# Kernel tuning notes

Hardware: AMD Instinct MI355X
Metric: run time of the kernel (lower is better)

## Reference

```python
import jax, jax.numpy as jnp
import numpy as np

B, C, H, W = 32, 1536, 24, 24
HID, D, K = 512, 128, 64  # hidden, cluster_dim, num_clusters


def setup_inputs() -> dict:
    key = jax.random.key(0)
    ks = jax.random.split(key, 6)
    def rn(k, shape, scale):
        return jax.random.normal(k, shape, dtype=jnp.float32) * scale
    return {
        "x": rn(ks[0], (B, C, H, W), 1.0),
        # cluster_features: Conv2d(C,512,1) -> ReLU -> Conv2d(512,D,1)
        "w1c": rn(ks[1], (HID, C), 0.02), "b1c": jnp.zeros((HID,), jnp.float32),
        "w2c": rn(ks[2], (D, HID), 0.02), "b2c": jnp.zeros((D,), jnp.float32),
        # score: Conv2d(C,512,1) -> ReLU -> Conv2d(512,K,1)
        "w1s": rn(ks[3], (HID, C), 0.02), "b1s": jnp.zeros((HID,), jnp.float32),
        "w2s": rn(ks[4], (K, HID), 0.02), "b2s": jnp.zeros((K,), jnp.float32),
        "temperature": jnp.array(1.0, jnp.float32),
    }


def _sinkhorn_log(S, num_iters=3):
    # log-domain OT solver with uniform marginals log(1/n), reg=1 (M/reg == M)
    b, m, n = S.shape
    norm = -jnp.log(jnp.asarray(n, S.dtype))
    log_a = jnp.full((b, m), norm, S.dtype)
    log_b = jnp.full((b, n), norm, S.dtype)
    u = jnp.zeros((b, m), S.dtype)
    v = jnp.zeros((b, n), S.dtype)
    for _ in range(num_iters):
        u = log_a - jax.nn.logsumexp(S + v[:, None, :], axis=2)
        v = log_b - jax.nn.logsumexp(S + u[:, :, None], axis=1)
    # get_matching_probs subtracts norm at the end
    return S + u[:, :, None] + v[:, None, :] - norm


def reference(x, w1c, b1c, w2c, b2c, w1s, b1s, w2s, b2s, temperature):
    b, c, h, w = x.shape
    xf = x.reshape(b, c, h * w)  # (B, C, N); 1x1 conv == channel GEMM
    # cluster features f: (B, D, N)
    hc = jax.nn.relu(jnp.einsum('oc,bcn->bon', w1c, xf) + b1c[None, :, None])
    f = jnp.einsum('oc,bcn->bon', w2c, hc) + b2c[None, :, None]
    # assignment scores p: (B, K, N)
    hs = jax.nn.relu(jnp.einsum('oc,bcn->bon', w1s, xf) + b1s[None, :, None])
    s = jnp.einsum('oc,bcn->bon', w2s, hs) + b2s[None, :, None]
    log_p = _sinkhorn_log(s, num_iters=3)
    p = jnp.exp(log_p / temperature) + jnp.exp(log_p)  # (B, K, N)
    # (f.unsqueeze(2) * p.unsqueeze(1)).sum(-1) == batched matmul
    agg = jnp.einsum('bcn,bkn->bck', f, p)  # (B, D, K)
    flat = agg.reshape(b, -1)
    nrm = jnp.maximum(jnp.linalg.norm(flat, axis=-1, keepdims=True), 1e-12)
    return flat / nrm
```

## Files before the change

### kernel.cpp

```cpp
#include <hip/hip_runtime.h>

typedef unsigned short ushort_t;
typedef float f32x4 __attribute__((ext_vector_type(4)));
typedef short short8 __attribute__((ext_vector_type(8)));

#define B_   32
#define C_   1536
#define N_   576
#define HID_ 512
#define D_   128
#define K_   64

__device__ __forceinline__ float bf2f(ushort_t u) {
    union { unsigned u; float f; } c; c.u = ((unsigned)u) << 16; return c.f;
}
__device__ __forceinline__ ushort_t f2bf(float x) {
    unsigned u = __float_as_uint(x);
    return (ushort_t)((u + 0x7FFFu + ((u >> 16) & 1u)) >> 16);
}

typedef const __attribute__((address_space(1))) char gas_char;
typedef __attribute__((address_space(3))) char las_char;
__device__ __forceinline__ void cp16(const void* g, void* l) {
    __builtin_amdgcn_global_load_lds((gas_char*)(size_t)g,
                                     (las_char*)(unsigned)(size_t)l, 16, 0, 0);
}
__device__ __forceinline__ void bar() {
    asm volatile("" ::: "memory");
    __builtin_amdgcn_s_barrier();
    asm volatile("" ::: "memory");
}

#define OB1_  1572864
#define OW2C_ 1573888
#define OB2C_ 1639424
#define OW2S_ 1639552
#define OB2S_ 1672320
#define WTOT_ 1672384
#define TRB_  6912
#define CVB4_ (((WTOT_ / 4) + 255) / 256)

__global__ __launch_bounds__(256) void prep_kernel(
    const void* __restrict__ x,
    const void* __restrict__ w1c, const void* __restrict__ b1c,
    const void* __restrict__ w2c, const void* __restrict__ b2c,
    const void* __restrict__ w1s, const void* __restrict__ b1s,
    const void* __restrict__ w2s, const void* __restrict__ b2s,
    const unsigned* __restrict__ temp,
    ushort_t* __restrict__ xt, ushort_t* __restrict__ o, float* __restrict__ Tp)
{
    __shared__ ushort_t t[64][68];
    unsigned d = temp[0];
    int flag = (d == 0x3F800000u) ? 1 : 0;
    int tid = threadIdx.x;
    int idx = blockIdx.x;
    if (idx == 0 && tid == 0)
        *Tp = flag ? __uint_as_float(d) : bf2f((ushort_t)(d & 0xFFFFu));

    if (idx < TRB_) {
        int b = idx / 216, rem = idx % 216;
        int c0 = (rem % 24) * 64, n0 = (rem / 24) * 64;
        ushort_t* xtb = xt + (size_t)b * N_ * C_;
        int r = tid >> 4, c4 = (tid & 15) * 4;
        if (flag) {
            const float* xb = (const float*)x + (size_t)b * C_ * N_;
#pragma unroll
            for (int i = 0; i < 4; ++i) {
                int cc = r + i * 16;
                float4 v = *(const float4*)&xb[(size_t)(c0 + cc) * N_ + n0 + c4];
                t[cc][c4 + 0] = f2bf(v.x);
                t[cc][c4 + 1] = f2bf(v.y);
                t[cc][c4 + 2] = f2bf(v.z);
                t[cc][c4 + 3] = f2bf(v.w);
            }
        } else {
            const ushort_t* xb = (const ushort_t*)x + (size_t)b * C_ * N_;
#pragma unroll
            for (int i = 0; i < 4; ++i) {
                int cc = r + i * 16;
                *(uint2*)&t[cc][c4] =
                    *(const uint2*)&xb[(size_t)(c0 + cc) * N_ + n0 + c4];
            }
        }
        __syncthreads();
#pragma unroll
        for (int i = 0; i < 4; ++i) {
            int nn = r + i * 16;
            ushort_t v0 = t[c4 + 0][nn], v1 = t[c4 + 1][nn];
            ushort_t v2 = t[c4 + 2][nn], v3 = t[c4 + 3][nn];
            uint2 vv;
            vv.x = (unsigned)v0 | ((unsigned)v1 << 16);
            vv.y = (unsigned)v2 | ((unsigned)v3 << 16);
            *(uint2*)&xtb[(size_t)(n0 + nn) * C_ + c0 + c4] = vv;
        }
    } else {
        int i4 = ((idx - TRB_) * 256 + tid) * 4;
        if (i4 >= WTOT_) return;
        const void* p; int off;
        if      (i4 < 786432)  { p = w1c; off = i4; }
        else if (i4 < OB1_)    { p = w1s; off = i4 - 786432; }
        else if (i4 < 1573376) { p = b1c; off = i4 - OB1_; }
        else if (i4 < OW2C_)   { p = b1s; off = i4 - 1573376; }
        else if (i4 < OB2C_)   { p = w2c; off = i4 - OW2C_; }
        else if (i4 < OW2S_)   { p = b2c; off = i4 - OB2C_; }
        else if (i4 < OB2S_)   { p = w2s; off = i4 - OW2S_; }
        else                   { p = b2s; off = i4 - OB2S_; }
        if (flag) {
            float4 v = *(const float4*)((const float*)p + off);
            uint2 r;
            r.x = (unsigned)f2bf(v.x) | ((unsigned)f2bf(v.y) << 16);
            r.y = (unsigned)f2bf(v.z) | ((unsigned)f2bf(v.w) << 16);
            *(uint2*)&o[i4] = r;
        } else {
            *(uint2*)&o[i4] = *(const uint2*)((const ushort_t*)p + off);
        }
    }
}

__global__ __launch_bounds__(256) void gemm1_kernel(
    const ushort_t* __restrict__ Xt, const ushort_t* __restrict__ W1,
    const ushort_t* __restrict__ bias, ushort_t* __restrict__ h)
{
    __shared__ ushort_t Atile[2][128 * 64];
    __shared__ ushort_t Btile[2][128 * 64];
    int idx = blockIdx.x;
    int l = (idx & 7) * 144 + (idx >> 3);
    int mt = l >> 3, t = l & 7;
    int row0 = mt * 128, col0 = t * 128;

    int tid = threadIdx.x, w = tid >> 6, lane = tid & 63;
    int wr = w >> 1, wc = w & 1;
    int r16 = lane & 15, q = lane >> 4, kh = q * 8;

    int srow = tid >> 3;
    int cx = ((tid & 7) ^ (srow & 7)) * 8;
    const ushort_t* ag[4];
    const ushort_t* bg[4];
#pragma unroll
    for (int s = 0; s < 4; ++s) {
        ag[s] = Xt + (size_t)(row0 + s * 32 + srow) * C_ + cx;
        bg[s] = W1 + (size_t)(col0 + s * 32 + srow) * C_ + cx;
    }

    f32x4 acc[4][4];
#pragma unroll
    for (int i = 0; i < 4; ++i)
#pragma unroll
        for (int j = 0; j < 4; ++j) acc[i][j] = f32x4{0.f, 0.f, 0.f, 0.f};

    int rowa = wr * 64 + r16;
    int rowb = wc * 64 + r16;
    int xr = (r16 & 7) * 8;

    auto stage = [&](int buf) {
#pragma unroll
        for (int s = 0; s < 4; ++s) {
            cp16(ag[s], &Atile[buf][tid * 8 + s * 2048]);
            cp16(bg[s], &Btile[buf][tid * 8 + s * 2048]);
            ag[s] += 64; bg[s] += 64;
        }
    };
    auto compute = [&](int cb) {
#pragma unroll
        for (int ks = 0; ks < 2; ++ks) {
            int ke = (ks * 32 + kh) ^ xr;
            short8 af[4], bf[4];
#pragma unroll
            for (int i = 0; i < 4; ++i)
                af[i] = *(const short8*)&Atile[cb][(rowa + i * 16) * 64 + ke];
#pragma unroll
            for (int j = 0; j < 4; ++j)
                bf[j] = *(const short8*)&Btile[cb][(rowb + j * 16) * 64 + ke];
#pragma unroll
            for (int i = 0; i < 4; ++i)
#pragma unroll
                for (int j = 0; j < 4; ++j)
                    acc[i][j] = __builtin_amdgcn_mfma_f32_16x16x32_bf16(
                        af[i], bf[j], acc[i][j], 0, 0, 0);
        }
    };

    stage(0);
    int cur = 0;
    for (int kt = 0; kt < 23; ++kt) {
        stage(cur ^ 1);
        asm volatile("s_waitcnt vmcnt(8)" ::: "memory");
        bar();
        compute(cur);
        bar();
        cur ^= 1;
    }
    asm volatile("s_waitcnt vmcnt(0)" ::: "memory");
    bar();
    compute(cur);

#pragma unroll
    for (int j = 0; j < 4; ++j) {
        int col = col0 + wc * 64 + j * 16 + r16;
        float cb = bf2f(bias[col]);
#pragma unroll
        for (int i = 0; i < 4; ++i) {
            int rowo = row0 + wr * 64 + i * 16 + q * 4;
#pragma unroll
            for (int r = 0; r < 4; ++r) {
                float v = fmaxf(acc[i][j][r] + cb, 0.f);
                h[(size_t)(rowo + r) * 1024 + col] = f2bf(v);
            }
        }
    }
}

__global__ __launch_bounds__(256) void gemm2_kernel(
    const ushort_t* __restrict__ Wb, const ushort_t* __restrict__ h,
    ushort_t* __restrict__ fbuf, float* __restrict__ sbuf)
{
    __shared__ ushort_t Atile[2][128 * 32];
    __shared__ ushort_t Btile[2][128 * 32];
    int nt = blockIdx.x, b = blockIdx.y, z = blockIdx.z;
    int col0 = nt * 128;
    int Mclamp = z ? K_ : D_;
    const ushort_t* Aw   = Wb + (z ? OW2S_ : OW2C_);
    const ushort_t* bias = Wb + (z ? OB2S_ : OB2C_);
    const ushort_t* hb = h + (size_t)b * N_ * 1024 + (z ? 512 : 0);

    int tid = threadIdx.x, w = tid >> 6, lane = tid & 63;
    int wr = w >> 1, wc = w & 1;
    int r16 = lane & 15, q = lane >> 4, kh = q * 8;

    int srow = tid >> 2;
    int swz = ((tid & 3) ^ (srow & 3)) * 8;
    int ar0 = min(srow, Mclamp - 1);
    int ar1 = min(64 + srow, Mclamp - 1);
    const ushort_t* ag0 = Aw + (size_t)ar0 * HID_ + swz;
    const ushort_t* ag1 = Aw + (size_t)ar1 * HID_ + swz;
    int br0 = min(col0 + srow, N_ - 1);
    int br1 = min(col0 + 64 + srow, N_ - 1);
    const ushort_t* bg0 = hb + (size_t)br0 * 1024 + swz;
    const ushort_t* bg1 = hb + (size_t)br1 * 1024 + swz;

    f32x4 acc[4][4];
#pragma unroll
    for (int i = 0; i < 4; ++i)
#pragma unroll
        for (int j = 0; j < 4; ++j) acc[i][j] = f32x4{0.f, 0.f, 0.f, 0.f};

    int xr = (r16 & 3) * 8;

    auto stage = [&](int buf) {
        cp16(ag0, &Atile[buf][tid * 8]);
        cp16(ag1, &Atile[buf][2048 + tid * 8]);
        cp16(bg0, &Btile[buf][tid * 8]);
        cp16(bg1, &Btile[buf][2048 + tid * 8]);
        ag0 += 32; ag1 += 32; bg0 += 32; bg1 += 32;
    };
    auto compute = [&](int cb) {
        int ke = kh ^ xr;
        short8 af[4], bf[4];
#pragma unroll
        for (int i = 0; i < 4; ++i)
            af[i] = *(const short8*)&Atile[cb][(wr * 64 + i * 16 + r16) * 32 + ke];
#pragma unroll
        for (int j = 0; j < 4; ++j)
            bf[j] = *(const short8*)&Btile[cb][(wc * 64 + j * 16 + r16) * 32 + ke];
#pragma unroll
        for (int i = 0; i < 4; ++i)
#pragma unroll
            for (int j = 0; j < 4; ++j)
                acc[i][j] = __builtin_amdgcn_mfma_f32_16x16x32_bf16(
                    af[i], bf[j], acc[i][j], 0, 0, 0);
    };

    stage(0);
    int cur = 0;
    for (int kt = 0; kt < 15; ++kt) {
        stage(cur ^ 1);
        asm volatile("s_waitcnt vmcnt(4)" ::: "memory");
        bar();
        compute(cur);
        bar();
        cur ^= 1;
    }
    asm volatile("s_waitcnt vmcnt(0)" ::: "memory");
    bar();
    compute(cur);

#pragma unroll
    for (int j = 0; j < 4; ++j) {
        int col = col0 + wc * 64 + j * 16 + r16;
#pragma unroll
        for (int i = 0; i < 4; ++i) {
            int rowb = wr * 64 + i * 16 + q * 4;
#pragma unroll
            for (int r = 0; r < 4; ++r) {
                int rr = rowb + r;
                if (rr < Mclamp && col < N_) {
                    float v = acc[i][j][r] + bf2f(bias[rr]);
                    if (z == 0)
                        fbuf[(size_t)b * D_ * N_ + (size_t)rr * N_ + col] = f2bf(v);
                    else
                        sbuf[(size_t)b * K_ * N_ + (size_t)rr * N_ + col] = v;
                }
            }
        }
    }
}

__global__ __launch_bounds__(512) void sinkhorn_kernel(
    const float* __restrict__ s_all, const float* __restrict__ Tp,
    ushort_t* __restrict__ P_all)
{
    int b = blockIdx.x;
    const float* S = s_all + (size_t)b * K_ * N_;
    __shared__ float Sl[K_ * 577];
    __shared__ float su[K_];
    __shared__ float sv[N_];
    int tid = threadIdx.x, w = tid >> 6, lane = tid & 63;
    const float norm = -logf((float)N_);

    const float4* S4 = (const float4*)S;
    for (int g = tid; g < (K_ * N_) / 4; g += 512) {
        float4 v = S4[g];
        int w0 = g * 4;
        int r = w0 / N_;
        int base = w0 + r;
        Sl[base + 0] = v.x; Sl[base + 1] = v.y;
        Sl[base + 2] = v.z; Sl[base + 3] = v.w;
    }
    for (int n = tid; n < N_; n += 512) sv[n] = 0.f;
    __syncthreads();

    for (int it = 0; it < 3; ++it) {
        for (int r = w; r < K_; r += 8) {
            const float* Sr = Sl + r * 577;
            float a0 = 0.f, a1 = 0.f, a2 = 0.f;
#pragma unroll
            for (int k = 0; k < 9; k += 3) {
                int n0 = lane + 64 * k;
                a0 += __expf(Sr[n0] + sv[n0]);
                a1 += __expf(Sr[n0 + 64] + sv[n0 + 64]);
                a2 += __expf(Sr[n0 + 128] + sv[n0 + 128]);
            }
            float t = a0 + a1 + a2;
#pragma unroll
            for (int off = 32; off; off >>= 1) t += __shfl_xor(t, off);
            if (lane == 0) su[r] = norm - __logf(t);
        }
        __syncthreads();
        for (int n = tid; n < N_; n += 512) {
            const float* Sc = Sl + n;
            float a0 = 0.f, a1 = 0.f, a2 = 0.f, a3 = 0.f;
#pragma unroll
            for (int m = 0; m < K_; m += 4) {
                a0 += __expf(Sc[(m + 0) * 577] + su[m + 0]);
                a1 += __expf(Sc[(m + 1) * 577] + su[m + 1]);
                a2 += __expf(Sc[(m + 2) * 577] + su[m + 2]);
                a3 += __expf(Sc[(m + 3) * 577] + su[m + 3]);
            }
            sv[n] = norm - __logf((a0 + a1) + (a2 + a3));
        }
        __syncthreads();
    }

    float invT = 1.f / (*Tp);
    ushort_t* Pb = P_all + (size_t)b * K_ * N_;
    for (int r = w; r < K_; r += 8) {
        float ur = su[r];
        const float* Sr = Sl + r * 577;
#pragma unroll
        for (int k = 0; k < 9; ++k) {
            int n0 = lane + 64 * k;
            float lp = Sr[n0] + ur + sv[n0] - norm;
            Pb[r * N_ + n0] = f2bf(__expf(lp * invT) + __expf(lp));
        }
    }
}

__global__ __launch_bounds__(256) void aggnorm_kernel(
    const ushort_t* __restrict__ f_all, const ushort_t* __restrict__ P_all,
    const unsigned* __restrict__ temp, void* __restrict__ out)
{
    __shared__ ushort_t Atile[2][128 * 64];
    __shared__ ushort_t Ptile[2][64 * 64];
    __shared__ float red[4];
    int b = blockIdx.x;
    const ushort_t* F = f_all + (size_t)b * D_ * N_;
    const ushort_t* P = P_all + (size_t)b * K_ * N_;
    int tid = threadIdx.x, w = tid >> 6, lane = tid & 63;
    int wr = w >> 1, wc = w & 1;
    int r16 = lane & 15, q = lane >> 4, kh = q * 8;

    int srow = tid >> 3;
    int cx = ((tid & 7) ^ (srow & 7)) * 8;
    const ushort_t* fg[4];
    const ushort_t* pg[2];
#pragma unroll
    for (int s = 0; s < 4; ++s)
        fg[s] = F + (size_t)(s * 32 + srow) * N_ + cx;
#pragma unroll
    for (int s = 0; s < 2; ++s)
        pg[s] = P + (size_t)(s * 32 + srow) * N_ + cx;

    f32x4 acc[4][2];
#pragma unroll
    for (int i = 0; i < 4; ++i)
#pragma unroll
        for (int j = 0; j < 2; ++j) acc[i][j] = f32x4{0.f, 0.f, 0.f, 0.f};

    int rowa = wr * 64 + r16;
    int rowp = wc * 32 + r16;
    int xr = (r16 & 7) * 8;

    auto stage = [&](int buf) {
#pragma unroll
        for (int s = 0; s < 4; ++s) {
            cp16(fg[s], &Atile[buf][tid * 8 + s * 2048]);
            fg[s] += 64;
        }
#pragma unroll
        for (int s = 0; s < 2; ++s) {
            cp16(pg[s], &Ptile[buf][tid * 8 + s * 2048]);
            pg[s] += 64;
        }
    };
    auto compute = [&](int cb) {
#pragma unroll
        for (int ks = 0; ks < 2; ++ks) {
            int ke = (ks * 32 + kh) ^ xr;
            short8 af[4], pf[2];
#pragma unroll
            for (int i = 0; i < 4; ++i)
                af[i] = *(const short8*)&Atile[cb][(rowa + i * 16) * 64 + ke];
#pragma unroll
            for (int j = 0; j < 2; ++j)
                pf[j] = *(const short8*)&Ptile[cb][(rowp + j * 16) * 64 + ke];
#pragma unroll
            for (int i = 0; i < 4; ++i)
#pragma unroll
                for (int j = 0; j < 2; ++j)
                    acc[i][j] = __builtin_amdgcn_mfma_f32_16x16x32_bf16(
                        af[i], pf[j], acc[i][j], 0, 0, 0);
        }
    };

    stage(0);
    int cur = 0;
    for (int kt = 0; kt < 8; ++kt) {
        stage(cur ^ 1);
        asm volatile("s_waitcnt vmcnt(6)" ::: "memory");
        bar();
        compute(cur);
        bar();
        cur ^= 1;
    }
    asm volatile("s_waitcnt vmcnt(0)" ::: "memory");
    bar();
    compute(cur);

    float ssq = 0.f;
#pragma unroll
    for (int i = 0; i < 4; ++i)
#pragma unroll
        for (int j = 0; j < 2; ++j)
#pragma unroll
            for (int r = 0; r < 4; ++r) { float v = acc[i][j][r]; ssq += v * v; }
#pragma unroll
    for (int off = 32; off; off >>= 1) ssq += __shfl_xor(ssq, off);
    if (lane == 0) red[w] = ssq;
    __syncthreads();
    float tot = red[0] + red[1] + red[2] + red[3];
    float inv = 1.f / fmaxf(sqrtf(tot), 1e-12f);
    int flag = (temp[0] == 0x3F800000u) ? 1 : 0;
#pragma unroll
    for (int i = 0; i < 4; ++i) {
#pragma unroll
        for (int j = 0; j < 2; ++j) {
            int col = wc * 32 + j * 16 + r16;
#pragma unroll
            for (int r = 0; r < 4; ++r) {
                int row = wr * 64 + i * 16 + q * 4 + r;
                float v = acc[i][j][r] * inv;
                size_t idx = (size_t)b * D_ * K_ + (size_t)row * K_ + col;
                if (flag) ((float*)out)[idx] = v;
                else      ((ushort_t*)out)[idx] = f2bf(v);
            }
        }
    }
}

extern "C" void kernel_launch(void* const* d_in, const int* in_sizes, int n_in,
                              void* d_out, int out_size, void* d_ws, size_t ws_size,
                              hipStream_t stream) {
    const void* x    = d_in[0];
    const void* w1c  = d_in[1];
    const void* b1c  = d_in[2];
    const void* w2c  = d_in[3];
    const void* b2c  = d_in[4];
    const void* w1s  = d_in[5];
    const void* b1s  = d_in[6];
    const void* w2s  = d_in[7];
    const void* b2s  = d_in[8];
    const unsigned* temp = (const unsigned*)d_in[9];

    char* ws = (char*)d_ws;
    float* Tp = (float*)ws;
    ushort_t* Wb = (ushort_t*)(ws + 256);
    size_t offXt = 256 + (((size_t)WTOT_ * 2 + 255) & ~(size_t)255);
    ushort_t* Xt = (ushort_t*)(ws + offXt);
    size_t xtBytes = (size_t)B_ * N_ * C_ * 2;
    ushort_t* h  = (ushort_t*)(ws + offXt + xtBytes);
    size_t o0 = offXt;
    ushort_t* fbuf = (ushort_t*)(ws + o0);  o0 += (size_t)B_ * D_ * N_ * 2;
    float*    sbuf = (float*)(ws + o0);     o0 += (size_t)B_ * K_ * N_ * 4;
    ushort_t* Pws  = (ushort_t*)(ws + o0);  o0 += (size_t)B_ * K_ * N_ * 2;

    prep_kernel<<<dim3(TRB_ + CVB4_), 256, 0, stream>>>(
        x, w1c, b1c, w2c, b2c, w1s, b1s, w2s, b2s, temp, Xt, Wb, Tp);
    gemm1_kernel<<<dim3(1152), 256, 0, stream>>>(Xt, Wb, Wb + OB1_, h);
    gemm2_kernel<<<dim3(5, B_, 2), 256, 0, stream>>>(Wb, h, fbuf, sbuf);
    sinkhorn_kernel<<<dim3(B_), 512, 0, stream>>>(sbuf, Tp, Pws);
    aggnorm_kernel<<<dim3(B_), 256, 0, stream>>>(fbuf, Pws, temp, (void*)d_out);
}
```

Measured before the change: 310.3 us.

## Widen transpose tiles to 128 channels and fully unroll GEMM K-loops with constant offsets

The prep transpose now handles 128x64 tiles per block. Stores go out as 16-byte uint4 writes instead of 8-byte ones, and the LDS row is padded to 65 elements. Separately, the pipelined K-loops in gemm1, gemm2 and aggnorm are fully unrolled, using compile-time offsets in place of pointer increments and a peeled last iteration. The aim is cheaper address math and better transpose store efficiency, at the cost of larger code size and odd-stride LDS access for ushorts.

```diff
diff --git a/kernel.cpp b/kernel.cpp
--- a/kernel.cpp
+++ b/kernel.cpp
@@ -37,7 +37,7 @@
 #define OW2S_ 1639552
 #define OB2S_ 1672320
 #define WTOT_ 1672384
-#define TRB_  6912
+#define TRB2_ 3456
 #define CVB4_ (((WTOT_ / 4) + 255) / 256)
 
 __global__ __launch_bounds__(256) void prep_kernel(
@@ -49,7 +49,7 @@
     const unsigned* __restrict__ temp,
     ushort_t* __restrict__ xt, ushort_t* __restrict__ o, float* __restrict__ Tp)
 {
-    __shared__ ushort_t t[64][68];
+    __shared__ ushort_t t[128][65];
     unsigned d = temp[0];
     int flag = (d == 0x3F800000u) ? 1 : 0;
     int tid = threadIdx.x;
@@ -57,44 +57,48 @@
     if (idx == 0 && tid == 0)
         *Tp = flag ? __uint_as_float(d) : bf2f((ushort_t)(d & 0xFFFFu));
 
-    if (idx < TRB_) {
-        int b = idx / 216, rem = idx % 216;
-        int c0 = (rem % 24) * 64, n0 = (rem / 24) * 64;
+    if (idx < TRB2_) {
+        int b = idx / 108, rem = idx % 108;
+        int c0 = (rem % 12) * 128, n0 = (rem / 12) * 64;
         ushort_t* xtb = xt + (size_t)b * N_ * C_;
-        int r = tid >> 4, c4 = (tid & 15) * 4;
+        int r = tid >> 4, n4 = (tid & 15) * 4;
         if (flag) {
             const float* xb = (const float*)x + (size_t)b * C_ * N_;
 #pragma unroll
-            for (int i = 0; i < 4; ++i) {
+            for (int i = 0; i < 8; ++i) {
                 int cc = r + i * 16;
-                float4 v = *(const float4*)&xb[(size_t)(c0 + cc) * N_ + n0 + c4];
-                t[cc][c4 + 0] = f2bf(v.x);
-                t[cc][c4 + 1] = f2bf(v.y);
-                t[cc][c4 + 2] = f2bf(v.z);
-                t[cc][c4 + 3] = f2bf(v.w);
+                float4 v = *(const float4*)&xb[(size_t)(c0 + cc) * N_ + n0 + n4];
+                t[cc][n4 + 0] = f2bf(v.x);
+                t[cc][n4 + 1] = f2bf(v.y);
+                t[cc][n4 + 2] = f2bf(v.z);
+                t[cc][n4 + 3] = f2bf(v.w);
             }
         } else {
             const ushort_t* xb = (const ushort_t*)x + (size_t)b * C_ * N_;
 #pragma unroll
-            for (int i = 0; i < 4; ++i) {
+            for (int i = 0; i < 8; ++i) {
                 int cc = r + i * 16;
-                *(uint2*)&t[cc][c4] =
-                    *(const uint2*)&xb[(size_t)(c0 + cc) * N_ + n0 + c4];
+                *(uint2*)&t[cc][n4] =
+                    *(const uint2*)&xb[(size_t)(c0 + cc) * N_ + n0 + n4];
             }
         }
         __syncthreads();
+        int c8 = (tid & 15) * 8;
 #pragma unroll
         for (int i = 0; i < 4; ++i) {
             int nn = r + i * 16;
-            ushort_t v0 = t[c4 + 0][nn], v1 = t[c4 + 1][nn];
-            ushort_t v2 = t[c4 + 2][nn], v3 = t[c4 + 3][nn];
-            uint2 vv;
-            vv.x = (unsigned)v0 | ((unsigned)v1 << 16);
-            vv.y = (unsigned)v2 | ((unsigned)v3 << 16);
-            *(uint2*)&xtb[(size_t)(n0 + nn) * C_ + c0 + c4] = vv;
+            ushort_t vv[8];
+#pragma unroll
+            for (int j = 0; j < 8; ++j) vv[j] = t[c8 + j][nn];
+            uint4 o4;
+            o4.x = (unsigned)vv[0] | ((unsigned)vv[1] << 16);
+            o4.y = (unsigned)vv[2] | ((unsigned)vv[3] << 16);
+            o4.z = (unsigned)vv[4] | ((unsigned)vv[5] << 16);
+            o4.w = (unsigned)vv[6] | ((unsigned)vv[7] << 16);
+            *(uint4*)&xtb[(size_t)(n0 + nn) * C_ + c0 + c8] = o4;
         }
     } else {
-        int i4 = ((idx - TRB_) * 256 + tid) * 4;
+        int i4 = ((idx - TRB2_) * 256 + tid) * 4;
         if (i4 >= WTOT_) return;
         const void* p; int off;
         if      (i4 < 786432)  { p = w1c; off = i4; }
@@ -152,12 +156,11 @@
     int rowb = wc * 64 + r16;
     int xr = (r16 & 7) * 8;
 
-    auto stage = [&](int buf) {
+    auto stage = [&](int buf, int koff) {
 #pragma unroll
         for (int s = 0; s < 4; ++s) {
-            cp16(ag[s], &Atile[buf][tid * 8 + s * 2048]);
-            cp16(bg[s], &Btile[buf][tid * 8 + s * 2048]);
-            ag[s] += 64; bg[s] += 64;
+            cp16(ag[s] + koff, &Atile[buf][tid * 8 + s * 2048]);
+            cp16(bg[s] + koff, &Btile[buf][tid * 8 + s * 2048]);
         }
     };
     auto compute = [&](int cb) {
@@ -180,19 +183,20 @@
         }
     };
 
-    stage(0);
-    int cur = 0;
-    for (int kt = 0; kt < 23; ++kt) {
-        stage(cur ^ 1);
-        asm volatile("s_waitcnt vmcnt(8)" ::: "memory");
+    stage(0, 0);
+#pragma unroll
+    for (int kt = 0; kt < 24; ++kt) {
+        int buf = kt & 1;
+        if (kt < 23) {
+            stage(buf ^ 1, (kt + 1) * 64);
+            asm volatile("s_waitcnt vmcnt(8)" ::: "memory");
+        } else {
+            asm volatile("s_waitcnt vmcnt(0)" ::: "memory");
+        }
         bar();
-        compute(cur);
+        compute(buf);
         bar();
-        cur ^= 1;
-    }
-    asm volatile("s_waitcnt vmcnt(0)" ::: "memory");
-    bar();
-    compute(cur);
+    }
 
 #pragma unroll
     for (int j = 0; j < 4; ++j) {
@@ -246,12 +250,11 @@
 
     int xr = (r16 & 3) * 8;
 
-    auto stage = [&](int buf) {
-        cp16(ag0, &Atile[buf][tid * 8]);
-        cp16(ag1, &Atile[buf][2048 + tid * 8]);
-        cp16(bg0, &Btile[buf][tid * 8]);
-        cp16(bg1, &Btile[buf][2048 + tid * 8]);
-        ag0 += 32; ag1 += 32; bg0 += 32; bg1 += 32;
+    auto stage = [&](int buf, int koff) {
+        cp16(ag0 + koff, &Atile[buf][tid * 8]);
+        cp16(ag1 + koff, &Atile[buf][2048 + tid * 8]);
+        cp16(bg0 + koff, &Btile[buf][tid * 8]);
+        cp16(bg1 + koff, &Btile[buf][2048 + tid * 8]);
     };
     auto compute = [&](int cb) {
         int ke = kh ^ xr;
@@ -270,19 +273,20 @@
                     af[i], bf[j], acc[i][j], 0, 0, 0);
     };
 
-    stage(0);
-    int cur = 0;
-    for (int kt = 0; kt < 15; ++kt) {
-        stage(cur ^ 1);
-        asm volatile("s_waitcnt vmcnt(4)" ::: "memory");
+    stage(0, 0);
+#pragma unroll
+    for (int kt = 0; kt < 16; ++kt) {
+        int buf = kt & 1;
+        if (kt < 15) {
+            stage(buf ^ 1, (kt + 1) * 32);
+            asm volatile("s_waitcnt vmcnt(4)" ::: "memory");
+        } else {
+            asm volatile("s_waitcnt vmcnt(0)" ::: "memory");
+        }
         bar();
-        compute(cur);
+        compute(buf);
         bar();
-        cur ^= 1;
-    }
-    asm volatile("s_waitcnt vmcnt(0)" ::: "memory");
-    bar();
-    compute(cur);
+    }
 
 #pragma unroll
     for (int j = 0; j < 4; ++j) {
@@ -410,17 +414,13 @@
     int rowp = wc * 32 + r16;
     int xr = (r16 & 7) * 8;
 
-    auto stage = [&](int buf) {
-#pragma unroll
-        for (int s = 0; s < 4; ++s) {
-            cp16(fg[s], &Atile[buf][tid * 8 + s * 2048]);
-            fg[s] += 64;
-        }
-#pragma unroll
-        for (int s = 0; s < 2; ++s) {
-            cp16(pg[s], &Ptile[buf][tid * 8 + s * 2048]);
-            pg[s] += 64;
-        }
+    auto stage = [&](int buf, int koff) {
+#pragma unroll
+        for (int s = 0; s < 4; ++s)
+            cp16(fg[s] + koff, &Atile[buf][tid * 8 + s * 2048]);
+#pragma unroll
+        for (int s = 0; s < 2; ++s)
+            cp16(pg[s] + koff, &Ptile[buf][tid * 8 + s * 2048]);
     };
     auto compute = [&](int cb) {
 #pragma unroll
@@ -442,19 +442,20 @@
         }
     };
 
-    stage(0);
-    int cur = 0;
-    for (int kt = 0; kt < 8; ++kt) {
-        stage(cur ^ 1);
-        asm volatile("s_waitcnt vmcnt(6)" ::: "memory");
+    stage(0, 0);
+#pragma unroll
+    for (int kt = 0; kt < 9; ++kt) {
+        int buf = kt & 1;
+        if (kt < 8) {
+            stage(buf ^ 1, (kt + 1) * 64);
+            asm volatile("s_waitcnt vmcnt(6)" ::: "memory");
+        } else {
+            asm volatile("s_waitcnt vmcnt(0)" ::: "memory");
+        }
         bar();
-        compute(cur);
+        compute(buf);
         bar();
-        cur ^= 1;
-    }
-    asm volatile("s_waitcnt vmcnt(0)" ::: "memory");
-    bar();
-    compute(cur);
+    }
 
     float ssq = 0.f;
 #pragma unroll
@@ -513,7 +514,7 @@
     float*    sbuf = (float*)(ws + o0);     o0 += (size_t)B_ * K_ * N_ * 4;
     ushort_t* Pws  = (ushort_t*)(ws + o0);  o0 += (size_t)B_ * K_ * N_ * 2;
 
-    prep_kernel<<<dim3(TRB_ + CVB4_), 256, 0, stream>>>(
+    prep_kernel<<<dim3(TRB2_ + CVB4_), 256, 0, stream>>>(
         x, w1c, b1c, w2c, b2c, w1s, b1s, w2s, b2s, temp, Xt, Wb, Tp);
     gemm1_kernel<<<dim3(1152), 256, 0, stream>>>(Xt, Wb, Wb + OB1_, h);
     gemm2_kernel<<<dim3(5, B_, 2), 256, 0, stream>>>(Wb, h, fbuf, sbuf);
```

Measured after the change: 302.4 us. 2.6% less time.
